# Optimization experiments

Measured on AMD Instinct MI355X. Metric: run time of the kernel, lower is better.

The kernel has to match this reference:

```python
import jax, jax.numpy as jnp
import numpy as np

E, K = 16, 4          # n_experts, top_k
C, H = 2048, 3584     # d_model, ffn_hidden
B, T = 2, 512
STD = 0.02


def setup_inputs() -> dict:
    key = jax.random.key(0)
    ks = jax.random.split(key, 5)
    x = jax.random.normal(ks[0], (B, T, C), jnp.float32)
    W_up = jax.random.normal(ks[1], (E, H, C), jnp.float32) * STD
    W_gate = jax.random.normal(ks[2], (E, H, C), jnp.float32) * STD
    W_down = jax.random.normal(ks[3], (E, C, H), jnp.float32) * STD
    gate_inp = jax.random.normal(ks[4], (E, C), jnp.float32) * STD
    return {"x": x, "W_up": W_up, "W_gate": W_gate, "W_down": W_down,
            "gate_inp": gate_inp}


def reference(x, W_up, W_gate, W_down, gate_inp):
    # x: [B, T, C]
    b, t, c = x.shape
    xf = x.reshape(b * t, c)                                  # [N, C]
    logits = xf @ gate_inp.T                                  # [N, E]
    topv, topi = jax.lax.top_k(logits, K)                     # [N, K]
    w = jax.nn.softmax(topv.astype(jnp.float32), axis=-1).astype(x.dtype)
    n = xf.shape[0]
    # Dense combine weights: zero for unselected experts -> identical math
    # to the original per-token gather, without the [N,K,H,C] blowup.
    dense_w = jnp.zeros((n, E), x.dtype).at[jnp.arange(n)[:, None], topi].set(w)
    u = jnp.einsum('nc,ehc->neh', xf, W_up)                   # [N, E, H]
    g = jnp.einsum('nc,ehc->neh', xf, W_gate)                 # [N, E, H]
    h = jax.nn.silu(g) * u                                    # SwiGLU
    y = jnp.einsum('neh,ech,ne->nc', h, W_down, dense_w)      # weighted combine
    return y.reshape(b, t, c)
```

## Files before the change

kernel.cpp:

```cpp
#include <hip/hip_runtime.h>
#include <math.h>

#define NTOK   1024
#define EXP    16
#define TOPK   4
#define DMODEL 2048
#define DFFN   3584
#define HT_TILES 56
#define CT_TILES 32
#define NSLOT  4096
#define NCHMAX 48

typedef __attribute__((ext_vector_type(8))) short bf16x8;
typedef __attribute__((ext_vector_type(4))) float f32x4;

#define O_COUNTS 0
#define O_BASE   256
#define O_CURSOR 512
#define O_CHT    1024
#define O_TOPI   4096
#define O_TOPW   (O_TOPI + 16384)
#define O_TOK    (O_TOPW + 16384)
#define O_WGT    (O_TOK + 16384)
#define O_SLOTNK (O_WGT + 16384)
#define O_XG     (O_SLOTNK + 16384)
#define O_HBUF   (O_XG + (size_t)NSLOT*DMODEL*2)

#define VMW(N) asm volatile("s_waitcnt vmcnt(" #N ")" ::: "memory")
#define LKW0() asm volatile("s_waitcnt lgkmcnt(0)" ::: "memory")
#define BAR()  __builtin_amdgcn_s_barrier()

__device__ __forceinline__ unsigned short f2b_rne(float f) {
  unsigned u = __builtin_bit_cast(unsigned, f);
  u += 0x7FFFu + ((u >> 16) & 1u);
  return (unsigned short)(u >> 16);
}
__device__ __forceinline__ float b2f(unsigned short h) {
  unsigned u = ((unsigned)h) << 16;
  return __builtin_bit_cast(float, u);
}
__device__ __forceinline__ unsigned pk2(float lo, float hi) {
  unsigned r;
  asm("v_cvt_pk_bf16_f32 %0, %1, %2" : "=v"(r) : "v"(lo), "v"(hi));
  return r;
}
__device__ __forceinline__ bf16x8 pack8(float4 a, float4 b) {
  union { unsigned u[4]; bf16x8 v; } r;
  r.u[0] = pk2(a.x, a.y); r.u[1] = pk2(a.z, a.w);
  r.u[2] = pk2(b.x, b.y); r.u[3] = pk2(b.z, b.w);
  return r.v;
}

__device__ __forceinline__ void gl16(const unsigned short* g, unsigned short* l) {
  __builtin_amdgcn_global_load_lds(
      (const __attribute__((address_space(1))) void*)g,
      (__attribute__((address_space(3))) void*)l, 16, 0, 0);
}

__device__ __forceinline__ bf16x8 ld_frag(const unsigned short* lds, int row, int chunk) {
  return *(const bf16x8*)(lds + row*64 + ((chunk ^ (row & 7)) * 8));
}

__global__ void k_zero(int* counts, int* cursor) {
  int t = threadIdx.x;
  if (t < EXP) { counts[t] = 0; cursor[t] = 0; }
}

__global__ void k_gate(const float* __restrict__ x, const float* __restrict__ gi,
                       int* __restrict__ topi, float* __restrict__ topw,
                       int* __restrict__ counts) {
  int n = blockIdx.x;
  int lane = threadIdx.x & 63, wave = threadIdx.x >> 6;
  __shared__ float lg[EXP];
  const float4* xr = (const float4*)(x + (size_t)n * DMODEL);
  #pragma unroll
  for (int i = 0; i < 4; ++i) {
    int e = wave * 4 + i;
    const float4* gr = (const float4*)(gi + (size_t)e * DMODEL);
    float s = 0.f;
    #pragma unroll
    for (int j = 0; j < 8; ++j) {
      float4 a = xr[j*64 + lane];
      float4 b = gr[j*64 + lane];
      s += a.x*b.x + a.y*b.y + a.z*b.z + a.w*b.w;
    }
    #pragma unroll
    for (int off = 32; off; off >>= 1) s += __shfl_xor(s, off);
    if (lane == 0) lg[e] = s;
  }
  __syncthreads();
  if (threadIdx.x == 0) {
    float v[EXP];
    #pragma unroll
    for (int j = 0; j < EXP; ++j) v[j] = lg[j];
    int bi[TOPK]; float bv[TOPK];
    #pragma unroll
    for (int k = 0; k < TOPK; ++k) {
      float best = -3.4e38f; int bidx = 0;
      for (int j = 0; j < EXP; ++j) if (v[j] > best) { best = v[j]; bidx = j; }
      bv[k] = best; bi[k] = bidx; v[bidx] = -3.4e38f;
    }
    float m = bv[0], ss = 0.f, w[TOPK];
    #pragma unroll
    for (int k = 0; k < TOPK; ++k) { w[k] = expf(bv[k] - m); ss += w[k]; }
    #pragma unroll
    for (int k = 0; k < TOPK; ++k) {
      topi[n*TOPK + k] = bi[k];
      topw[n*TOPK + k] = w[k] / ss;
      atomicAdd(&counts[bi[k]], 1);
    }
  }
}

__global__ void k_prefix(const int* __restrict__ counts, int* __restrict__ basep,
                         int* __restrict__ chtab) {
  if (threadIdx.x == 0) {
    int acc = 0;
    for (int e = 0; e < EXP; ++e) { basep[e] = acc; acc += counts[e]; }
    int c = 0;
    for (int e = 0; e < EXP; ++e) {
      int nm = (counts[e] + 127) >> 7;
      for (int m = 0; m < nm; ++m) { chtab[1 + c] = (e << 8) | m; ++c; }
    }
    chtab[0] = c;
    for (; c < NCHMAX; ++c) chtab[1 + c] = -1;
  }
}

__global__ void k_scatter(const int* __restrict__ topi, const float* __restrict__ topw,
                          const int* __restrict__ basep, int* __restrict__ cursor,
                          int* __restrict__ tok, float* __restrict__ wgt,
                          int* __restrict__ slotnk) {
  int n = blockIdx.x * blockDim.x + threadIdx.x;
  if (n >= NTOK) return;
  #pragma unroll
  for (int k = 0; k < TOPK; ++k) {
    int e = topi[n*TOPK + k];
    int pos = atomicAdd(&cursor[e], 1);
    int slot = basep[e] + pos;
    tok[slot] = n;
    wgt[slot] = topw[n*TOPK + k];
    slotnk[n*TOPK + k] = slot;
  }
}

__global__ void k_gather(const float* __restrict__ x, const int* __restrict__ tok,
                         unsigned short* __restrict__ xg) {
  int slot = blockIdx.x;
  int t = tok[slot];
  int c0 = threadIdx.x * 8;
  const float* src = x + (size_t)t * DMODEL + c0;
  float4 a = *(const float4*)(src);
  float4 b = *(const float4*)(src + 4);
  uint4 o = {pk2(a.x, a.y), pk2(a.z, a.w), pk2(b.x, b.y), pk2(b.z, b.w)};
  *(uint4*)(xg + (size_t)slot * DMODEL + c0) = o;
}

#define UG_STEP(XSC, XSN, PC, PN, KC) do {                                     \
    BAR();                                                                     \
    int kn_ = (KC) + 1; if (kn_ > DMODEL/64 - 1) kn_ = DMODEL/64 - 1;          \
    const float* pu_ = wu_row + kn_*64;                                        \
    const float* pg_ = wg_row + kn_*64;                                        \
    float4 r0_ = *(const float4*)(pu_);                                        \
    float4 r1_ = *(const float4*)(pu_ + 4);                                    \
    float4 r2_ = *(const float4*)(pu_ + 32);                                   \
    float4 r3_ = *(const float4*)(pu_ + 36);                                   \
    float4 r4_ = *(const float4*)(pg_);                                        \
    float4 r5_ = *(const float4*)(pg_ + 4);                                    \
    float4 r6_ = *(const float4*)(pg_ + 32);                                   \
    float4 r7_ = *(const float4*)(pg_ + 36);                                   \
    _Pragma("unroll")                                                          \
    for (int i_ = 0; i_ < 4; ++i_)                                             \
      gl16(bx[i_] + kn_*64, (XSN) + (i_*4 + wave)*8*64);                       \
    VMW(12);                                                                   \
    BAR();                                                                     \
    _Pragma("unroll")                                                          \
    for (int kk_ = 0; kk_ < 2; ++kk_) {                                        \
      int chunk_ = kk_*4 + (lane >> 4);                                        \
      _Pragma("unroll")                                                        \
      for (int t_ = 0; t_ < 8; ++t_) {                                         \
        bf16x8 a_ = ld_frag((XSC), t_*16 + col, chunk_);                       \
        ua[t_] = __builtin_amdgcn_mfma_f32_16x16x32_bf16(a_, PC[kk_],   ua[t_], 0, 0, 0); \
        ga[t_] = __builtin_amdgcn_mfma_f32_16x16x32_bf16(a_, PC[2+kk_], ga[t_], 0, 0, 0); \
      }                                                                        \
    }                                                                          \
    VMW(4);                                                                    \
    PN[0] = pack8(r0_, r1_); PN[1] = pack8(r2_, r3_);                          \
    PN[2] = pack8(r4_, r5_); PN[3] = pack8(r6_, r7_);                          \
  } while (0)

__global__ __launch_bounds__(256, 3) void k_upgate(
    const unsigned short* __restrict__ xg,
    const float* __restrict__ Wu, const float* __restrict__ Wg,
    const int* __restrict__ counts, const int* __restrict__ basep,
    const int* __restrict__ chtab, const float* __restrict__ wgt,
    unsigned short* __restrict__ hbuf) {
  int bid = blockIdx.x;
  int lb  = (bid & 7) * (NCHMAX*HT_TILES/8) + (bid >> 3);
  int cid = lb % NCHMAX, ht = lb / NCHMAX;
  int ent = chtab[1 + cid];
  if (ent < 0) return;
  int e = ent >> 8, mch = ent & 255;
  int n_e = counts[e], base_e = basep[e], mstart = mch * 128;

  __shared__ unsigned short xs[2][128*64];
  __shared__ float swgt[128];

  int tid = threadIdx.x;
  int lane = tid & 63, wave = tid >> 6;
  int col = lane & 15;
  int kgrp = (lane >> 4) * 8;
  const float* wu_row = Wu + ((size_t)e * DFFN + (size_t)(ht*64 + wave*16 + col)) * DMODEL + kgrp;
  const float* wg_row = Wg + ((size_t)e * DFFN + (size_t)(ht*64 + wave*16 + col)) * DMODEL + kgrp;

  int xrow_lo = lane >> 3;
  int xpc     = lane & 7;
  int swz     = (xpc ^ xrow_lo) * 8;

  const unsigned short* bx[4];
  #pragma unroll
  for (int i = 0; i < 4; ++i) {
    int row = (i*4 + wave)*8 + xrow_lo;
    int slotr = base_e + mstart + row;
    if (slotr > NSLOT-1) slotr = NSLOT-1;
    bx[i] = xg + (size_t)slotr*DMODEL + swz;
  }

  if (tid < 128) {
    int r = mstart + tid;
    swgt[tid] = (r < n_e) ? wgt[base_e + r] : 0.f;
  }
  LKW0();

  bf16x8 pA[4], pB[4];
  {
    const float* pu_ = wu_row;
    const float* pg_ = wg_row;
    float4 r0 = *(const float4*)(pu_);
    float4 r1 = *(const float4*)(pu_ + 4);
    float4 r2 = *(const float4*)(pu_ + 32);
    float4 r3 = *(const float4*)(pu_ + 36);
    float4 r4 = *(const float4*)(pg_);
    float4 r5 = *(const float4*)(pg_ + 4);
    float4 r6 = *(const float4*)(pg_ + 32);
    float4 r7 = *(const float4*)(pg_ + 36);
    #pragma unroll
    for (int i = 0; i < 4; ++i)
      gl16(bx[i], &xs[0][(i*4 + wave)*8*64]);
    VMW(4);
    pA[0] = pack8(r0, r1); pA[1] = pack8(r2, r3);
    pA[2] = pack8(r4, r5); pA[3] = pack8(r6, r7);
  }

  f32x4 ua[8], ga[8];
  #pragma unroll
  for (int t = 0; t < 8; ++t) { f32x4 z = {0.f,0.f,0.f,0.f}; ua[t] = z; ga[t] = z; }

  #pragma unroll 1
  for (int kc = 0; kc < DMODEL/64; kc += 2) {
    UG_STEP(xs[0], xs[1], pA, pB, kc);
    UG_STEP(xs[1], xs[0], pB, pA, kc + 1);
  }

  #pragma unroll
  for (int t = 0; t < 8; ++t)
    #pragma unroll
    for (int r = 0; r < 4; ++r) {
      int ml = t*16 + (lane >> 4)*4 + r;
      if (mstart + ml < n_e) {
        float u = ua[t][r], g = ga[t][r];
        float hv = u * (g / (1.f + expf(-g))) * swgt[ml];
        int slot = base_e + mstart + ml;
        hbuf[(size_t)slot*DFFN + ht*64 + wave*16 + col] = f2b_rne(hv);
      }
    }
}

#define DN_STEP(XSC, XSN, PC, PN, KC) do {                                     \
    BAR();                                                                     \
    int kn_ = (KC) + 1; if (kn_ > DFFN/64 - 1) kn_ = DFFN/64 - 1;              \
    const float* pd_ = wd_row + kn_*64;                                        \
    float4 r0_ = *(const float4*)(pd_);                                        \
    float4 r1_ = *(const float4*)(pd_ + 4);                                    \
    float4 r2_ = *(const float4*)(pd_ + 32);                                   \
    float4 r3_ = *(const float4*)(pd_ + 36);                                   \
    _Pragma("unroll")                                                          \
    for (int i_ = 0; i_ < 4; ++i_)                                             \
      gl16(bh[i_] + kn_*64, (XSN) + (i_*4 + wave)*8*64);                       \
    VMW(8);                                                                    \
    BAR();                                                                     \
    _Pragma("unroll")                                                          \
    for (int kk_ = 0; kk_ < 2; ++kk_) {                                        \
      int chunk_ = kk_*4 + (lane >> 4);                                        \
      _Pragma("unroll")                                                        \
      for (int t_ = 0; t_ < 8; ++t_) {                                         \
        bf16x8 a_ = ld_frag((XSC), t_*16 + col, chunk_);                       \
        acc[t_] = __builtin_amdgcn_mfma_f32_16x16x32_bf16(a_, PC[kk_], acc[t_], 0, 0, 0); \
      }                                                                        \
    }                                                                          \
    VMW(4);                                                                    \
    PN[0] = pack8(r0_, r1_); PN[1] = pack8(r2_, r3_);                          \
  } while (0)

__global__ __launch_bounds__(256, 4) void k_down(
    const unsigned short* __restrict__ hbuf, const float* __restrict__ Wd,
    const int* __restrict__ counts, const int* __restrict__ basep,
    const int* __restrict__ chtab,
    unsigned short* __restrict__ ypart) {
  int bid = blockIdx.x;
  int lb  = (bid & 7) * (NCHMAX*CT_TILES/8) + (bid >> 3);
  int cid = lb % NCHMAX, ct = lb / NCHMAX;
  int ent = chtab[1 + cid];
  if (ent < 0) return;
  int e = ent >> 8, mch = ent & 255;
  int n_e = counts[e], base_e = basep[e], mstart = mch * 128;

  __shared__ unsigned short hs[2][128*64];

  int tid = threadIdx.x;
  int lane = tid & 63, wave = tid >> 6;
  int col = lane & 15;
  int kgrp = (lane >> 4) * 8;
  const float* wd_row = Wd + ((size_t)e * DMODEL + (size_t)(ct*64 + wave*16 + col)) * DFFN + kgrp;

  int xrow_lo = lane >> 3;
  int xpc     = lane & 7;
  int swz     = (xpc ^ xrow_lo) * 8;

  const unsigned short* bh[4];
  #pragma unroll
  for (int i = 0; i < 4; ++i) {
    int row = (i*4 + wave)*8 + xrow_lo;
    int slotr = base_e + mstart + row;
    if (slotr > NSLOT-1) slotr = NSLOT-1;
    bh[i] = hbuf + (size_t)slotr*DFFN + swz;
  }

  bf16x8 pA[2], pB[2];
  {
    const float* pd_ = wd_row;
    float4 r0 = *(const float4*)(pd_);
    float4 r1 = *(const float4*)(pd_ + 4);
    float4 r2 = *(const float4*)(pd_ + 32);
    float4 r3 = *(const float4*)(pd_ + 36);
    #pragma unroll
    for (int i = 0; i < 4; ++i)
      gl16(bh[i], &hs[0][(i*4 + wave)*8*64]);
    VMW(4);
    pA[0] = pack8(r0, r1); pA[1] = pack8(r2, r3);
  }

  f32x4 acc[8];
  #pragma unroll
  for (int t = 0; t < 8; ++t) { f32x4 z = {0.f,0.f,0.f,0.f}; acc[t] = z; }

  #pragma unroll 1
  for (int hc = 0; hc < DFFN/64; hc += 2) {
    DN_STEP(hs[0], hs[1], pA, pB, hc);
    DN_STEP(hs[1], hs[0], pB, pA, hc + 1);
  }

  #pragma unroll
  for (int t = 0; t < 8; ++t)
    #pragma unroll
    for (int r = 0; r < 4; ++r) {
      int ml = t*16 + (lane >> 4)*4 + r;
      if (mstart + ml < n_e) {
        int slot = base_e + mstart + ml;
        ypart[(size_t)slot*DMODEL + ct*64 + wave*16 + col] = f2b_rne(acc[t][r]);
      }
    }
}

__global__ void k_combine(const unsigned short* __restrict__ ypart,
                          const int* __restrict__ slotnk, float* __restrict__ out) {
  int n = blockIdx.x, tid = threadIdx.x;
  int c0 = tid * 8;
  float acc[8] = {0.f,0.f,0.f,0.f,0.f,0.f,0.f,0.f};
  #pragma unroll
  for (int k = 0; k < TOPK; ++k) {
    int slot = slotnk[n*TOPK + k];
    uint4 v = *(const uint4*)(ypart + (size_t)slot*DMODEL + c0);
    const unsigned short* p = (const unsigned short*)&v;
    #pragma unroll
    for (int j = 0; j < 8; ++j) acc[j] += b2f(p[j]);
  }
  float4 o0 = {acc[0], acc[1], acc[2], acc[3]};
  float4 o1 = {acc[4], acc[5], acc[6], acc[7]};
  *(float4*)(out + (size_t)n*DMODEL + c0)     = o0;
  *(float4*)(out + (size_t)n*DMODEL + c0 + 4) = o1;
}

extern "C" void kernel_launch(void* const* d_in, const int* in_sizes, int n_in,
                              void* d_out, int out_size, void* d_ws, size_t ws_size,
                              hipStream_t stream) {
  const float* x     = (const float*)d_in[0];
  const float* W_up  = (const float*)d_in[1];
  const float* W_gt  = (const float*)d_in[2];
  const float* W_dn  = (const float*)d_in[3];
  const float* g_in  = (const float*)d_in[4];
  float* out = (float*)d_out;
  char* ws = (char*)d_ws;

  int*   counts = (int*)(ws + O_COUNTS);
  int*   basep  = (int*)(ws + O_BASE);
  int*   cursor = (int*)(ws + O_CURSOR);
  int*   chtab  = (int*)(ws + O_CHT);
  int*   topi   = (int*)(ws + O_TOPI);
  float* topw   = (float*)(ws + O_TOPW);
  int*   tok    = (int*)(ws + O_TOK);
  float* wgt    = (float*)(ws + O_WGT);
  int*   slotnk = (int*)(ws + O_SLOTNK);
  unsigned short* xg    = (unsigned short*)(ws + O_XG);
  unsigned short* hbuf  = (unsigned short*)(ws + O_HBUF);
  unsigned short* ypart = xg;

  k_zero   <<<1, 64, 0, stream>>>(counts, cursor);
  k_gate   <<<NTOK, 256, 0, stream>>>(x, g_in, topi, topw, counts);
  k_prefix <<<1, 64, 0, stream>>>(counts, basep, chtab);
  k_scatter<<<4, 256, 0, stream>>>(topi, topw, basep, cursor, tok, wgt, slotnk);
  k_gather <<<NSLOT, 256, 0, stream>>>(x, tok, xg);
  k_upgate <<<NCHMAX*HT_TILES, 256, 0, stream>>>(xg, W_up, W_gt, counts, basep, chtab, wgt, hbuf);
  k_down   <<<NCHMAX*CT_TILES, 256, 0, stream>>>(hbuf, W_dn, counts, basep, chtab, ypart);
  k_combine<<<NTOK, 256, 0, stream>>>(ypart, slotnk, out);
}
```

Measured before the change: 772.3 us.

## Triple-buffer activation tiles and prefetch two steps ahead in MoE GEMMs

```diff
diff --git a/kernel.cpp b/kernel.cpp
--- a/kernel.cpp
+++ b/kernel.cpp
@@ -9,6 +9,7 @@
 #define HT_TILES 56
 #define CT_TILES 32
 #define NSLOT  4096
+#define MCH    128
 #define NCHMAX 48
 
 typedef __attribute__((ext_vector_type(8))) short bf16x8;
@@ -119,7 +120,7 @@
     for (int e = 0; e < EXP; ++e) { basep[e] = acc; acc += counts[e]; }
     int c = 0;
     for (int e = 0; e < EXP; ++e) {
-      int nm = (counts[e] + 127) >> 7;
+      int nm = (counts[e] + MCH - 1) / MCH;
       for (int m = 0; m < nm; ++m) { chtab[1 + c] = (e << 8) | m; ++c; }
     }
     chtab[0] = c;
@@ -156,37 +157,37 @@
   *(uint4*)(xg + (size_t)slot * DMODEL + c0) = o;
 }
 
-#define UG_STEP(XSC, XSN, PC, PN, KC) do {                                     \
+#define UG_STEP(PC, PN, KC, CUR) do {                                          \
+    VMW(12);                                                                   \
     BAR();                                                                     \
-    int kn_ = (KC) + 1; if (kn_ > DMODEL/64 - 1) kn_ = DMODEL/64 - 1;          \
+    VMW(4);                                                                    \
+    PN[0] = pack8(rw0, rw1); PN[1] = pack8(rw2, rw3);                          \
+    PN[2] = pack8(rw4, rw5); PN[3] = pack8(rw6, rw7);                          \
+    int kn_ = (KC) + 2; if (kn_ > DMODEL/64 - 1) kn_ = DMODEL/64 - 1;          \
     const float* pu_ = wu_row + kn_*64;                                        \
     const float* pg_ = wg_row + kn_*64;                                        \
-    float4 r0_ = *(const float4*)(pu_);                                        \
-    float4 r1_ = *(const float4*)(pu_ + 4);                                    \
-    float4 r2_ = *(const float4*)(pu_ + 32);                                   \
-    float4 r3_ = *(const float4*)(pu_ + 36);                                   \
-    float4 r4_ = *(const float4*)(pg_);                                        \
-    float4 r5_ = *(const float4*)(pg_ + 4);                                    \
-    float4 r6_ = *(const float4*)(pg_ + 32);                                   \
-    float4 r7_ = *(const float4*)(pg_ + 36);                                   \
+    rw0 = *(const float4*)(pu_);      rw1 = *(const float4*)(pu_ + 4);         \
+    rw2 = *(const float4*)(pu_ + 32); rw3 = *(const float4*)(pu_ + 36);        \
+    rw4 = *(const float4*)(pg_);      rw5 = *(const float4*)(pg_ + 4);         \
+    rw6 = *(const float4*)(pg_ + 32); rw7 = *(const float4*)(pg_ + 36);        \
+    int wb_ = (CUR) + 2; if (wb_ >= 3) wb_ -= 3;                               \
+    unsigned short* xw_ = xs + wb_*8192;                                       \
     _Pragma("unroll")                                                          \
     for (int i_ = 0; i_ < 4; ++i_)                                             \
-      gl16(bx[i_] + kn_*64, (XSN) + (i_*4 + wave)*8*64);                       \
-    VMW(12);                                                                   \
-    BAR();                                                                     \
+      gl16(bx[i_] + kn_*64, xw_ + (i_*4 + wave)*8*64);                         \
+    const unsigned short* xr_ = xs + (CUR)*8192;                               \
+    __builtin_amdgcn_s_setprio(1);                                             \
     _Pragma("unroll")                                                          \
     for (int kk_ = 0; kk_ < 2; ++kk_) {                                        \
       int chunk_ = kk_*4 + (lane >> 4);                                        \
       _Pragma("unroll")                                                        \
       for (int t_ = 0; t_ < 8; ++t_) {                                         \
-        bf16x8 a_ = ld_frag((XSC), t_*16 + col, chunk_);                       \
+        bf16x8 a_ = ld_frag(xr_, t_*16 + col, chunk_);                         \
         ua[t_] = __builtin_amdgcn_mfma_f32_16x16x32_bf16(a_, PC[kk_],   ua[t_], 0, 0, 0); \
         ga[t_] = __builtin_amdgcn_mfma_f32_16x16x32_bf16(a_, PC[2+kk_], ga[t_], 0, 0, 0); \
       }                                                                        \
     }                                                                          \
-    VMW(4);                                                                    \
-    PN[0] = pack8(r0_, r1_); PN[1] = pack8(r2_, r3_);                          \
-    PN[2] = pack8(r4_, r5_); PN[3] = pack8(r6_, r7_);                          \
+    __builtin_amdgcn_s_setprio(0);                                             \
   } while (0)
 
 __global__ __launch_bounds__(256, 3) void k_upgate(
@@ -197,14 +198,14 @@
     unsigned short* __restrict__ hbuf) {
   int bid = blockIdx.x;
   int lb  = (bid & 7) * (NCHMAX*HT_TILES/8) + (bid >> 3);
-  int cid = lb % NCHMAX, ht = lb / NCHMAX;
+  int cid = lb / HT_TILES, ht = lb % HT_TILES;
   int ent = chtab[1 + cid];
   if (ent < 0) return;
   int e = ent >> 8, mch = ent & 255;
-  int n_e = counts[e], base_e = basep[e], mstart = mch * 128;
-
-  __shared__ unsigned short xs[2][128*64];
-  __shared__ float swgt[128];
+  int n_e = counts[e], base_e = basep[e], mstart = mch * MCH;
+
+  __shared__ unsigned short xs[3*8192];
+  __shared__ float swgt[MCH];
 
   int tid = threadIdx.x;
   int lane = tid & 63, wave = tid >> 6;
@@ -226,40 +227,40 @@
     bx[i] = xg + (size_t)slotr*DMODEL + swz;
   }
 
-  if (tid < 128) {
+  if (tid < MCH) {
     int r = mstart + tid;
     swgt[tid] = (r < n_e) ? wgt[base_e + r] : 0.f;
   }
   LKW0();
 
+  float4 rw0, rw1, rw2, rw3, rw4, rw5, rw6, rw7;
   bf16x8 pA[4], pB[4];
-  {
-    const float* pu_ = wu_row;
-    const float* pg_ = wg_row;
-    float4 r0 = *(const float4*)(pu_);
-    float4 r1 = *(const float4*)(pu_ + 4);
-    float4 r2 = *(const float4*)(pu_ + 32);
-    float4 r3 = *(const float4*)(pu_ + 36);
-    float4 r4 = *(const float4*)(pg_);
-    float4 r5 = *(const float4*)(pg_ + 4);
-    float4 r6 = *(const float4*)(pg_ + 32);
-    float4 r7 = *(const float4*)(pg_ + 36);
-    #pragma unroll
-    for (int i = 0; i < 4; ++i)
-      gl16(bx[i], &xs[0][(i*4 + wave)*8*64]);
-    VMW(4);
-    pA[0] = pack8(r0, r1); pA[1] = pack8(r2, r3);
-    pA[2] = pack8(r4, r5); pA[3] = pack8(r6, r7);
-  }
+
+  rw0 = *(const float4*)(wu_row);      rw1 = *(const float4*)(wu_row + 4);
+  rw2 = *(const float4*)(wu_row + 32); rw3 = *(const float4*)(wu_row + 36);
+  rw4 = *(const float4*)(wg_row);      rw5 = *(const float4*)(wg_row + 4);
+  rw6 = *(const float4*)(wg_row + 32); rw7 = *(const float4*)(wg_row + 36);
+  #pragma unroll
+  for (int i = 0; i < 4; ++i) gl16(bx[i],        xs        + (i*4 + wave)*8*64);
+  #pragma unroll
+  for (int i = 0; i < 4; ++i) gl16(bx[i] + 64,   xs + 8192 + (i*4 + wave)*8*64);
+  VMW(8);
+  pA[0] = pack8(rw0, rw1); pA[1] = pack8(rw2, rw3);
+  pA[2] = pack8(rw4, rw5); pA[3] = pack8(rw6, rw7);
+  rw0 = *(const float4*)(wu_row + 64);      rw1 = *(const float4*)(wu_row + 68);
+  rw2 = *(const float4*)(wu_row + 96);      rw3 = *(const float4*)(wu_row + 100);
+  rw4 = *(const float4*)(wg_row + 64);      rw5 = *(const float4*)(wg_row + 68);
+  rw6 = *(const float4*)(wg_row + 96);      rw7 = *(const float4*)(wg_row + 100);
 
   f32x4 ua[8], ga[8];
   #pragma unroll
   for (int t = 0; t < 8; ++t) { f32x4 z = {0.f,0.f,0.f,0.f}; ua[t] = z; ga[t] = z; }
 
+  int cur = 0;
   #pragma unroll 1
   for (int kc = 0; kc < DMODEL/64; kc += 2) {
-    UG_STEP(xs[0], xs[1], pA, pB, kc);
-    UG_STEP(xs[1], xs[0], pB, pA, kc + 1);
+    UG_STEP(pA, pB, kc, cur);     cur = (cur == 2) ? 0 : cur + 1;
+    UG_STEP(pB, pA, kc + 1, cur); cur = (cur == 2) ? 0 : cur + 1;
   }
 
   #pragma unroll
@@ -276,46 +277,48 @@
     }
 }
 
-#define DN_STEP(XSC, XSN, PC, PN, KC) do {                                     \
+#define DN_STEP(PC, PN, KC, CUR) do {                                          \
+    VMW(8);                                                                    \
     BAR();                                                                     \
-    int kn_ = (KC) + 1; if (kn_ > DFFN/64 - 1) kn_ = DFFN/64 - 1;              \
+    VMW(4);                                                                    \
+    PN[0] = pack8(rw0, rw1); PN[1] = pack8(rw2, rw3);                          \
+    int kn_ = (KC) + 2; if (kn_ > DFFN/64 - 1) kn_ = DFFN/64 - 1;              \
     const float* pd_ = wd_row + kn_*64;                                        \
-    float4 r0_ = *(const float4*)(pd_);                                        \
-    float4 r1_ = *(const float4*)(pd_ + 4);                                    \
-    float4 r2_ = *(const float4*)(pd_ + 32);                                   \
-    float4 r3_ = *(const float4*)(pd_ + 36);                                   \
+    rw0 = *(const float4*)(pd_);      rw1 = *(const float4*)(pd_ + 4);         \
+    rw2 = *(const float4*)(pd_ + 32); rw3 = *(const float4*)(pd_ + 36);        \
+    int wb_ = (CUR) + 2; if (wb_ >= 3) wb_ -= 3;                               \
+    unsigned short* xw_ = hs + wb_*8192;                                       \
     _Pragma("unroll")                                                          \
     for (int i_ = 0; i_ < 4; ++i_)                                             \
-      gl16(bh[i_] + kn_*64, (XSN) + (i_*4 + wave)*8*64);                       \
-    VMW(8);                                                                    \
-    BAR();                                                                     \
+      gl16(bh[i_] + kn_*64, xw_ + (i_*4 + wave)*8*64);                         \
+    const unsigned short* xr_ = hs + (CUR)*8192;                               \
+    __builtin_amdgcn_s_setprio(1);                                             \
     _Pragma("unroll")                                                          \
     for (int kk_ = 0; kk_ < 2; ++kk_) {                                        \
       int chunk_ = kk_*4 + (lane >> 4);                                        \
       _Pragma("unroll")                                                        \
       for (int t_ = 0; t_ < 8; ++t_) {                                         \
-        bf16x8 a_ = ld_frag((XSC), t_*16 + col, chunk_);                       \
+        bf16x8 a_ = ld_frag(xr_, t_*16 + col, chunk_);                         \
         acc[t_] = __builtin_amdgcn_mfma_f32_16x16x32_bf16(a_, PC[kk_], acc[t_], 0, 0, 0); \
       }                                                                        \
     }                                                                          \
-    VMW(4);                                                                    \
-    PN[0] = pack8(r0_, r1_); PN[1] = pack8(r2_, r3_);                          \
+    __builtin_amdgcn_s_setprio(0);                                             \
   } while (0)
 
-__global__ __launch_bounds__(256, 4) void k_down(
+__global__ __launch_bounds__(256, 3) void k_down(
     const unsigned short* __restrict__ hbuf, const float* __restrict__ Wd,
     const int* __restrict__ counts, const int* __restrict__ basep,
     const int* __restrict__ chtab,
     unsigned short* __restrict__ ypart) {
   int bid = blockIdx.x;
   int lb  = (bid & 7) * (NCHMAX*CT_TILES/8) + (bid >> 3);
-  int cid = lb % NCHMAX, ct = lb / NCHMAX;
+  int cid = lb / CT_TILES, ct = lb % CT_TILES;
   int ent = chtab[1 + cid];
   if (ent < 0) return;
   int e = ent >> 8, mch = ent & 255;
-  int n_e = counts[e], base_e = basep[e], mstart = mch * 128;
-
-  __shared__ unsigned short hs[2][128*64];
+  int n_e = counts[e], base_e = basep[e], mstart = mch * MCH;
+
+  __shared__ unsigned short hs[3*8192];
 
   int tid = threadIdx.x;
   int lane = tid & 63, wave = tid >> 6;
@@ -336,28 +339,29 @@
     bh[i] = hbuf + (size_t)slotr*DFFN + swz;
   }
 
+  float4 rw0, rw1, rw2, rw3;
   bf16x8 pA[2], pB[2];
-  {
-    const float* pd_ = wd_row;
-    float4 r0 = *(const float4*)(pd_);
-    float4 r1 = *(const float4*)(pd_ + 4);
-    float4 r2 = *(const float4*)(pd_ + 32);
-    float4 r3 = *(const float4*)(pd_ + 36);
-    #pragma unroll
-    for (int i = 0; i < 4; ++i)
-      gl16(bh[i], &hs[0][(i*4 + wave)*8*64]);
-    VMW(4);
-    pA[0] = pack8(r0, r1); pA[1] = pack8(r2, r3);
-  }
+
+  rw0 = *(const float4*)(wd_row);      rw1 = *(const float4*)(wd_row + 4);
+  rw2 = *(const float4*)(wd_row + 32); rw3 = *(const float4*)(wd_row + 36);
+  #pragma unroll
+  for (int i = 0; i < 4; ++i) gl16(bh[i],      hs        + (i*4 + wave)*8*64);
+  #pragma unroll
+  for (int i = 0; i < 4; ++i) gl16(bh[i] + 64, hs + 8192 + (i*4 + wave)*8*64);
+  VMW(8);
+  pA[0] = pack8(rw0, rw1); pA[1] = pack8(rw2, rw3);
+  rw0 = *(const float4*)(wd_row + 64); rw1 = *(const float4*)(wd_row + 68);
+  rw2 = *(const float4*)(wd_row + 96); rw3 = *(const float4*)(wd_row + 100);
 
   f32x4 acc[8];
   #pragma unroll
   for (int t = 0; t < 8; ++t) { f32x4 z = {0.f,0.f,0.f,0.f}; acc[t] = z; }
 
+  int cur = 0;
   #pragma unroll 1
   for (int hc = 0; hc < DFFN/64; hc += 2) {
-    DN_STEP(hs[0], hs[1], pA, pB, hc);
-    DN_STEP(hs[1], hs[0], pB, pA, hc + 1);
+    DN_STEP(pA, pB, hc, cur);     cur = (cur == 2) ? 0 : cur + 1;
+    DN_STEP(pB, pA, hc + 1, cur); cur = (cur == 2) ? 0 : cur + 1;
   }
 
   #pragma unroll
```

Result: slower. 964.6 us (+24.9%).
